# Kernel optimization log

Measured on AMD Instinct MI355X. Metric: run time of the kernel, lower is better.

Reference implementation:

```python
import jax, jax.numpy as jnp
import numpy as np

HIDDEN = 32


def setup_inputs() -> dict:
    key = jax.random.key(0)
    ks = jax.random.split(key, 8)
    B, T, I = 1024, 512, 64
    s_ih = 1.0 / np.sqrt(HIDDEN)
    return {
        "x": jax.random.normal(ks[0], (B, T, I), dtype=jnp.float32),
        "h0": jnp.zeros((1, B, HIDDEN), dtype=jnp.float32),
        "W_ih": jax.random.uniform(ks[1], (HIDDEN, I), jnp.float32, -s_ih, s_ih),
        "b_ih": jax.random.uniform(ks[2], (HIDDEN,), jnp.float32, -s_ih, s_ih),
        "W_hh": jax.random.uniform(ks[3], (HIDDEN, HIDDEN), jnp.float32, -s_ih, s_ih),
        "b_hh": jax.random.uniform(ks[4], (HIDDEN,), jnp.float32, -s_ih, s_ih),
        "W_out": jax.random.uniform(ks[5], (1, HIDDEN), jnp.float32, -s_ih, s_ih),
        "b_out": jax.random.uniform(ks[6], (1,), jnp.float32, -s_ih, s_ih),
    }


def reference(x, h0, W_ih, b_ih, W_hh, b_hh, W_out, b_out):
    # x: [B, T, I]; h0: [1, B, H] (num_layers=1)
    # Precompute input contribution for all timesteps in one GEMM: [B, T, H]
    x_proj = jnp.einsum("bti,hi->bth", x, W_ih) + b_ih

    def step(h, xt):  # h: [B, H], xt: [B, H]
        h_new = jnp.tanh(xt + h @ W_hh.T + b_hh)
        return h_new, h_new

    h_last, r_out_t = jax.lax.scan(step, h0[0], jnp.swapaxes(x_proj, 0, 1))
    r_out = jnp.swapaxes(r_out_t, 0, 1)  # [B, T, H]
    # Per-timestep Linear(32 -> 1), batched as one GEMM: [B, T, 1]
    outs = r_out @ W_out.T + b_out
    return outs, h_last[None]
```

## Files before the change

### kernel.cpp

```cpp
#include <hip/hip_runtime.h>

#define Bc 1024
#define Tc 512
#define Ic 64
#define Hc 32
#define XP 516

typedef __bf16 bf16x8 __attribute__((ext_vector_type(8)));
typedef __bf16 bf16x4 __attribute__((ext_vector_type(4)));
typedef float  f32x4  __attribute__((ext_vector_type(4)));

__device__ inline bf16x8 to_bf16x8(float4 u0, float4 u1) {
    bf16x8 t;
    t[0] = (__bf16)u0.x; t[1] = (__bf16)u0.y; t[2] = (__bf16)u0.z; t[3] = (__bf16)u0.w;
    t[4] = (__bf16)u1.x; t[5] = (__bf16)u1.y; t[6] = (__bf16)u1.z; t[7] = (__bf16)u1.w;
    return t;
}

#define RWC(hvv, wvv)                                                         \
    a0 = fmaf((hvv).x, (wvv).x, a0);                                          \
    a1 = fmaf((hvv).y, (wvv).y, a1);                                          \
    a2 = fmaf((hvv).z, (wvv).z, a2);                                          \
    a3 = fmaf((hvv).w, (wvv).w, a3);

#define STEP(xval, uu)                                                        \
    {                                                                         \
        hbuf[half][h] = hval;                                                 \
        __builtin_amdgcn_wave_barrier();                                      \
        const float4* hv = (const float4*)hbuf[half];                         \
        const float4 h0v = hv[0], h1v = hv[1], h2v = hv[2], h3v = hv[3],      \
                     h4v = hv[4], h5v = hv[5], h6v = hv[6], h7v = hv[7];      \
        float a0 = (xval) + bias, a1 = 0.f, a2 = 0.f, a3 = 0.f;               \
        RWC(h0v, w0) RWC(h1v, w1) RWC(h2v, w2) RWC(h3v, w3)                   \
        RWC(h4v, w4) RWC(h5v, w5) RWC(h6v, w6) RWC(h7v, w7)                   \
        const float a = (a0 + a1) + (a2 + a3);                                \
        const float p  = __builtin_amdgcn_exp2f(a * 2.8853900817779268f);     \
        const float rr = __builtin_amdgcn_rcpf(p + 1.0f);                     \
        hval = fmaf(-2.0f, rr, 1.0f);                                         \
        pbuf[half][uu][h] = wo * hval;                                        \
        __builtin_amdgcn_wave_barrier();                                      \
    }

#define CVT4(dst, src)                                                        \
    dst.x = (float)(src)[0]; dst.y = (float)(src)[1];                         \
    dst.z = (float)(src)[2]; dst.w = (float)(src)[3];

__global__ __launch_bounds__(64) void fused_rnn_kernel(
    const float* __restrict__ x, const float* __restrict__ Wih,
    const float* __restrict__ bih, const float* __restrict__ h0,
    const float* __restrict__ Whh, const float* __restrict__ bhh,
    const float* __restrict__ Wout, const float* __restrict__ bout,
    float* __restrict__ out)
{
    __shared__ __bf16 xq[2][Hc][XP];
    __shared__ float hbuf[2][32];
    __shared__ float pbuf[2][16][34];

    const int lane = threadIdx.x;
    const int half = lane >> 5;
    const int h    = lane & 31;
    const int m    = lane & 15;
    const int q    = lane >> 4;
    const int b0   = blockIdx.x * 2;

    bf16x8 Bf[2][2];
#pragma unroll
    for (int nh = 0; nh < 2; ++nh)
#pragma unroll
        for (int kh = 0; kh < 2; ++kh) {
            const float* wp = Wih + (m + 16 * nh) * Ic + q * 8 + kh * 32;
            Bf[nh][kh] = to_bf16x8(((const float4*)wp)[0], ((const float4*)wp)[1]);
        }
    const float bias0 = bih[m];
    const float bias1 = bih[m + 16];

#pragma unroll 4
    for (int tt = 0; tt < 64; ++tt) {
        const int bb = tt >> 5;
        const int lt = tt & 31;
        const float* xp0 =
            x + ((size_t)(b0 + bb) * Tc + lt * 16 + m) * Ic + q * 8;
        const bf16x8 A0 = to_bf16x8(((const float4*)xp0)[0],
                                    ((const float4*)xp0)[1]);
        const bf16x8 A1 = to_bf16x8(((const float4*)(xp0 + 32))[0],
                                    ((const float4*)(xp0 + 32))[1]);

        f32x4 acc0 = {0.f, 0.f, 0.f, 0.f};
        f32x4 acc1 = {0.f, 0.f, 0.f, 0.f};
        acc0 = __builtin_amdgcn_mfma_f32_16x16x32_bf16(A0, Bf[0][0], acc0, 0, 0, 0);
        acc0 = __builtin_amdgcn_mfma_f32_16x16x32_bf16(A1, Bf[0][1], acc0, 0, 0, 0);
        acc1 = __builtin_amdgcn_mfma_f32_16x16x32_bf16(A0, Bf[1][0], acc1, 0, 0, 0);
        acc1 = __builtin_amdgcn_mfma_f32_16x16x32_bf16(A1, Bf[1][1], acc1, 0, 0, 0);

        bf16x4 p0, p1;
        p0[0] = (__bf16)(acc0[0] + bias0); p0[1] = (__bf16)(acc0[1] + bias0);
        p0[2] = (__bf16)(acc0[2] + bias0); p0[3] = (__bf16)(acc0[3] + bias0);
        p1[0] = (__bf16)(acc1[0] + bias1); p1[1] = (__bf16)(acc1[1] + bias1);
        p1[2] = (__bf16)(acc1[2] + bias1); p1[3] = (__bf16)(acc1[3] + bias1);
        *(bf16x4*)&xq[bb][m][lt * 16 + q * 4]      = p0;
        *(bf16x4*)&xq[bb][m + 16][lt * 16 + q * 4] = p1;
    }

    __syncthreads();

    const float4* wrow = (const float4*)(Whh + h * Hc);
    const float4 w0 = wrow[0], w1 = wrow[1], w2 = wrow[2], w3 = wrow[3],
                 w4 = wrow[4], w5 = wrow[5], w6 = wrow[6], w7 = wrow[7];
    const float bias = bhh[h];
    const float wo   = Wout[h];
    const float bo   = bout[0];

    float hval = h0[(size_t)(b0 + half) * Hc + h];
    float* orow = out + (size_t)(b0 + half) * Tc;

    const __bf16* xrow = &xq[half][h][0];

    bf16x4 r0 = *(const bf16x4*)(xrow + 0), r1 = *(const bf16x4*)(xrow + 4),
           r2 = *(const bf16x4*)(xrow + 8), r3 = *(const bf16x4*)(xrow + 12);
    float4 q0, q1, q2, q3;
    CVT4(q0, r0) CVT4(q1, r1) CVT4(q2, r2) CVT4(q3, r3)

    for (int tb = 0; tb < Tc / 16; ++tb) {
        const int tbn = (tb + 1 < Tc / 16) ? tb + 1 : tb;
        const __bf16* nx = xrow + tbn * 16;
        const bf16x4 m0 = *(const bf16x4*)(nx + 0),
                     m1 = *(const bf16x4*)(nx + 4),
                     m2 = *(const bf16x4*)(nx + 8),
                     m3 = *(const bf16x4*)(nx + 12);

        STEP(q0.x, 0)  STEP(q0.y, 1)  STEP(q0.z, 2)  STEP(q0.w, 3)
        STEP(q1.x, 4)  STEP(q1.y, 5)  STEP(q1.z, 6)  STEP(q1.w, 7)
        STEP(q2.x, 8)  STEP(q2.y, 9)  STEP(q2.z, 10) STEP(q2.w, 11)
        STEP(q3.x, 12) STEP(q3.y, 13) STEP(q3.z, 14) STEP(q3.w, 15)

        __builtin_amdgcn_wave_barrier();

        if (h < 16) {
            const float2* pr = (const float2*)pbuf[half][h];
            float2 sa = pr[0], sb = pr[1];
#pragma unroll
            for (int mm = 2; mm < 16; mm += 2) {
                sa.x += pr[mm].x;     sa.y += pr[mm].y;
                sb.x += pr[mm + 1].x; sb.y += pr[mm + 1].y;
            }
            orow[tb * 16 + h] = ((sa.x + sb.x) + (sa.y + sb.y)) + bo;
        }
        __builtin_amdgcn_wave_barrier();

        CVT4(q0, m0) CVT4(q1, m1) CVT4(q2, m2) CVT4(q3, m3)
    }

    out[(size_t)Bc * Tc + (size_t)(b0 + half) * Hc + h] = hval;
}

extern "C" void kernel_launch(void* const* d_in, const int* in_sizes, int n_in,
                              void* d_out, int out_size, void* d_ws, size_t ws_size,
                              hipStream_t stream) {
    const float* x    = (const float*)d_in[0];
    const float* h0   = (const float*)d_in[1];
    const float* Wih  = (const float*)d_in[2];
    const float* bih  = (const float*)d_in[3];
    const float* Whh  = (const float*)d_in[4];
    const float* bhh  = (const float*)d_in[5];
    const float* Wout = (const float*)d_in[6];
    const float* bout = (const float*)d_in[7];
    float* out = (float*)d_out;

    fused_rnn_kernel<<<Bc / 2, 64, 0, stream>>>(x, Wih, bih, h0, Whh, bhh,
                                                Wout, bout, out);
}
```

Before: 275.5 us.

## Warp-specialize RNN: MFMA recurrence over 16 batches with producer wave for input projection

Replaces the scalar per-lane recurrence (two batches per block, FMA dot products through LDS) with a two-wave design. One wave runs the hidden-state recurrence for 16 batch rows as f16 MFMAs, using a sigmoid reformulation of tanh and permlane swaps to rebuild the B operand in registers. The other wave streams x, computes the input projection with bf16 MFMAs into a triple-buffered LDS ring and writes the reduced outputs. This targets the serial per-step latency and the low occupancy of the old layout, at the cost of f16 precision in the recurrence and one block-wide barrier per 8 timesteps.

```diff
diff --git a/kernel.cpp b/kernel.cpp
--- a/kernel.cpp
+++ b/kernel.cpp
@@ -4,11 +4,17 @@
 #define Tc 512
 #define Ic 64
 #define Hc 32
-#define XP 516
-
-typedef __bf16 bf16x8 __attribute__((ext_vector_type(8)));
-typedef __bf16 bf16x4 __attribute__((ext_vector_type(4)));
-typedef float  f32x4  __attribute__((ext_vector_type(4)));
+#define NB 16
+#define TT 8
+#define NT (Tc / TT)
+#define XP2 36
+#define L2E2 2.8853900817779268f
+
+typedef __bf16   bf16x8 __attribute__((ext_vector_type(8)));
+typedef _Float16 half8  __attribute__((ext_vector_type(8)));
+typedef float    f32x4  __attribute__((ext_vector_type(4)));
+typedef unsigned u32x4  __attribute__((ext_vector_type(4)));
+typedef unsigned uint2v __attribute__((ext_vector_type(2)));
 
 __device__ inline bf16x8 to_bf16x8(float4 u0, float4 u1) {
     bf16x8 t;
@@ -16,141 +22,279 @@
     t[4] = (__bf16)u1.x; t[5] = (__bf16)u1.y; t[6] = (__bf16)u1.z; t[7] = (__bf16)u1.w;
     return t;
 }
-
-#define RWC(hvv, wvv)                                                         \
-    a0 = fmaf((hvv).x, (wvv).x, a0);                                          \
-    a1 = fmaf((hvv).y, (wvv).y, a1);                                          \
-    a2 = fmaf((hvv).z, (wvv).z, a2);                                          \
-    a3 = fmaf((hvv).w, (wvv).w, a3);
-
-#define STEP(xval, uu)                                                        \
+__device__ inline bf16x8 to_bf16x8s(float4 u0, float4 u1, float s) {
+    bf16x8 t;
+    t[0] = (__bf16)(u0.x*s); t[1] = (__bf16)(u0.y*s); t[2] = (__bf16)(u0.z*s); t[3] = (__bf16)(u0.w*s);
+    t[4] = (__bf16)(u1.x*s); t[5] = (__bf16)(u1.y*s); t[6] = (__bf16)(u1.z*s); t[7] = (__bf16)(u1.w*s);
+    return t;
+}
+
+
+#if __has_builtin(__builtin_amdgcn_permlane16_swap)
+#define PLSWAP(A, B)                                                          \
+    { uint2v _t = __builtin_amdgcn_permlane16_swap((A), (B), false, false);   \
+      (A) = _t[0]; (B) = _t[1]; }
+#else
+#define PLSWAP(A, B)                                                          \
+    asm("s_nop 1\n\tv_permlane16_swap_b32 %0, %1" : "+v"(A), "+v"(B));
+#endif
+#if __has_builtin(__builtin_amdgcn_permlane32_swap)
+#define P32SWAP(A, B)                                                         \
+    { uint2v _t = __builtin_amdgcn_permlane32_swap((A), (B), false, false);   \
+      (A) = _t[0]; (B) = _t[1]; }
+#else
+#define P32SWAP(A, B)                                                         \
+    asm("s_nop 1\n\tv_permlane32_swap_b32 %0, %1" : "+v"(A), "+v"(B));
+#endif
+
+#define RSW16(X, OUT) { unsigned a__=(X), b__=(X); PLSWAP(a__,b__); OUT = ps16 ? a__ : b__; }
+#define RSW32(X, OUT) { unsigned a__=(X), b__=(X); P32SWAP(a__,b__); OUT = ps32 ? a__ : b__; }
+
+#define PK(a, b) __builtin_bit_cast(unsigned, __builtin_amdgcn_cvt_pkrtz((a), (b)))
+
+#define SSTEP(CC1, CC2, CN1, CN2, uu, tpf, upf)                               \
     {                                                                         \
-        hbuf[half][h] = hval;                                                 \
-        __builtin_amdgcn_wave_barrier();                                      \
-        const float4* hv = (const float4*)hbuf[half];                         \
-        const float4 h0v = hv[0], h1v = hv[1], h2v = hv[2], h3v = hv[3],      \
-                     h4v = hv[4], h5v = hv[5], h6v = hv[6], h7v = hv[7];      \
-        float a0 = (xval) + bias, a1 = 0.f, a2 = 0.f, a3 = 0.f;               \
-        RWC(h0v, w0) RWC(h1v, w1) RWC(h2v, w2) RWC(h3v, w3)                   \
-        RWC(h4v, w4) RWC(h5v, w5) RWC(h6v, w6) RWC(h7v, w7)                   \
-        const float a = (a0 + a1) + (a2 + a3);                                \
-        const float p  = __builtin_amdgcn_exp2f(a * 2.8853900817779268f);     \
-        const float rr = __builtin_amdgcn_rcpf(p + 1.0f);                     \
-        hval = fmaf(-2.0f, rr, 1.0f);                                         \
-        pbuf[half][uu][h] = wo * hval;                                        \
-        __builtin_amdgcn_wave_barrier();                                      \
-    }
-
-#define CVT4(dst, src)                                                        \
-    dst.x = (float)(src)[0]; dst.y = (float)(src)[1];                         \
-    dst.z = (float)(src)[2]; dst.w = (float)(src)[3];
-
-__global__ __launch_bounds__(64) void fused_rnn_kernel(
+        const float* pf_ = xqlds + (((tpf) % 3) * TT + (upf)) * (NB * XP2)    \
+                           + n * XP2 + 4 * q;                                 \
+        CN1 = *(const f32x4*)pf_;                                             \
+        CN2 = *(const f32x4*)(pf_ + 16);                                      \
+        const f32x4 D1_ = __builtin_amdgcn_mfma_f32_16x16x32_f16(A1f, Bst, CC1, 0, 0, 0); \
+        const f32x4 D2_ = __builtin_amdgcn_mfma_f32_16x16x32_f16(A2f, Bst, CC2, 0, 0, 0); \
+        r10 = __builtin_amdgcn_rcpf(__builtin_amdgcn_exp2f(D1_[0]) + 1.0f);   \
+        r11 = __builtin_amdgcn_rcpf(__builtin_amdgcn_exp2f(D1_[1]) + 1.0f);   \
+        r12 = __builtin_amdgcn_rcpf(__builtin_amdgcn_exp2f(D1_[2]) + 1.0f);   \
+        r13 = __builtin_amdgcn_rcpf(__builtin_amdgcn_exp2f(D1_[3]) + 1.0f);   \
+        r20 = __builtin_amdgcn_rcpf(__builtin_amdgcn_exp2f(D2_[0]) + 1.0f);   \
+        r21 = __builtin_amdgcn_rcpf(__builtin_amdgcn_exp2f(D2_[1]) + 1.0f);   \
+        r22 = __builtin_amdgcn_rcpf(__builtin_amdgcn_exp2f(D2_[2]) + 1.0f);   \
+        r23 = __builtin_amdgcn_rcpf(__builtin_amdgcn_exp2f(D2_[3]) + 1.0f);   \
+        const unsigned G0_ = PK(r10, r20), G1_ = PK(r11, r21);                \
+        const unsigned G2_ = PK(r12, r22), G3_ = PK(r13, r23);                \
+        unsigned B1_, B2_, B3_;                                               \
+        RSW16(G1_, B1_) RSW32(G2_, B2_) RSW16(G3_, B3_)                       \
+        u32x4 bu_; bu_[0] = G0_; bu_[1] = B1_; bu_[2] = B2_; bu_[3] = B3_;    \
+        Bst = __builtin_bit_cast(half8, bu_);                                 \
+        pbuf[(((tb & 1) * TT + (uu)) * NB + n) * 4 + q] =                     \
+            fmaf(r10, w2a0, fmaf(r11, w2a1, fmaf(r12, w2a2, fmaf(r13, w2a3,  \
+            fmaf(r20, w2b0, fmaf(r21, w2b1, fmaf(r22, w2b2, r23 * w2b3)))))));\
+    }
+
+#define XDECL(S) float4 X##S##0, X##S##1, X##S##2, X##S##3;
+
+#define HLOAD(S, wt)                                                          \
+    if ((wt) < Tc) {                                                          \
+        const float* xp_ = x + ((size_t)(b0 + n) * Tc + (wt)) * Ic + q * 8;   \
+        X##S##0 = ((const float4*)xp_)[0];                                    \
+        X##S##1 = ((const float4*)xp_)[1];                                    \
+        X##S##2 = ((const float4*)(xp_ + 32))[0];                             \
+        X##S##3 = ((const float4*)(xp_ + 32))[1];                             \
+    }
+
+#define HMFMA(S, wt)                                                          \
+    if ((wt) < Tc) {                                                          \
+        const bf16x8 A0_ = to_bf16x8(X##S##0, X##S##1);                       \
+        const bf16x8 A1_ = to_bf16x8(X##S##2, X##S##3);                       \
+        f32x4 d1_ = CbH1, d2_ = CbH2;                                         \
+        d1_ = __builtin_amdgcn_mfma_f32_16x16x32_bf16(A0_, Pw00, d1_, 0,0,0); \
+        d1_ = __builtin_amdgcn_mfma_f32_16x16x32_bf16(A1_, Pw01, d1_, 0,0,0); \
+        d2_ = __builtin_amdgcn_mfma_f32_16x16x32_bf16(A0_, Pw10, d2_, 0,0,0); \
+        d2_ = __builtin_amdgcn_mfma_f32_16x16x32_bf16(A1_, Pw11, d2_, 0,0,0); \
+        float* wb_ = xqlds + ((((wt) >> 3) % 3) * TT + ((wt) & 7)) * (NB * XP2); \
+        wb_[(4*q + 0) * XP2 + n]      = d1_[0];                               \
+        wb_[(4*q + 1) * XP2 + n]      = d1_[1];                               \
+        wb_[(4*q + 2) * XP2 + n]      = d1_[2];                               \
+        wb_[(4*q + 3) * XP2 + n]      = d1_[3];                               \
+        wb_[(4*q + 0) * XP2 + n + 16] = d2_[0];                               \
+        wb_[(4*q + 1) * XP2 + n + 16] = d2_[1];                               \
+        wb_[(4*q + 2) * XP2 + n + 16] = d2_[2];                               \
+        wb_[(4*q + 3) * XP2 + n + 16] = d2_[3];                               \
+    }
+
+#define HSTEP(S, wt, wtn) HMFMA(S, wt) HLOAD(S, wtn)
+
+#define HRED(tbr)                                                             \
+    {                                                                         \
+        const int n2_ = lane >> 2, ug_ = (lane & 3) * 2;                      \
+        const float* pr_ = pbuf + ((((tbr) & 1) * TT + ug_) * NB + n2_) * 4;  \
+        const f32x4 pa_ = *(const f32x4*)pr_;                                 \
+        const f32x4 pb_ = *(const f32x4*)(pr_ + NB * 4);                      \
+        float2 sv_;                                                           \
+        sv_.x = ((pa_[0] + pa_[1]) + (pa_[2] + pa_[3])) + cst;                \
+        sv_.y = ((pb_[0] + pb_[1]) + (pb_[2] + pb_[3])) + cst;                \
+        *(float2*)(out + (size_t)(b0 + n2_) * Tc + (tbr) * TT + ug_) = sv_;   \
+    }
+
+__global__ __launch_bounds__(128, 1) void fused_rnn_kernel(
     const float* __restrict__ x, const float* __restrict__ Wih,
     const float* __restrict__ bih, const float* __restrict__ h0,
     const float* __restrict__ Whh, const float* __restrict__ bhh,
     const float* __restrict__ Wout, const float* __restrict__ bout,
     float* __restrict__ out)
 {
-    __shared__ __bf16 xq[2][Hc][XP];
-    __shared__ float hbuf[2][32];
-    __shared__ float pbuf[2][16][34];
-
-    const int lane = threadIdx.x;
-    const int half = lane >> 5;
-    const int h    = lane & 31;
-    const int m    = lane & 15;
+    __shared__ float xqlds[3 * TT * NB * XP2];
+    __shared__ float pbuf[2 * TT * NB * 4];
+
+    const int tid  = threadIdx.x;
+    const int wid  = tid >> 6;
+    const int lane = tid & 63;
+    const int n    = lane & 15;
     const int q    = lane >> 4;
-    const int b0   = blockIdx.x * 2;
-
-    bf16x8 Bf[2][2];
-#pragma unroll
-    for (int nh = 0; nh < 2; ++nh)
-#pragma unroll
-        for (int kh = 0; kh < 2; ++kh) {
-            const float* wp = Wih + (m + 16 * nh) * Ic + q * 8 + kh * 32;
-            Bf[nh][kh] = to_bf16x8(((const float4*)wp)[0], ((const float4*)wp)[1]);
-        }
-    const float bias0 = bih[m];
-    const float bias1 = bih[m + 16];
-
-#pragma unroll 4
-    for (int tt = 0; tt < 64; ++tt) {
-        const int bb = tt >> 5;
-        const int lt = tt & 31;
-        const float* xp0 =
-            x + ((size_t)(b0 + bb) * Tc + lt * 16 + m) * Ic + q * 8;
-        const bf16x8 A0 = to_bf16x8(((const float4*)xp0)[0],
-                                    ((const float4*)xp0)[1]);
-        const bf16x8 A1 = to_bf16x8(((const float4*)(xp0 + 32))[0],
-                                    ((const float4*)(xp0 + 32))[1]);
-
-        f32x4 acc0 = {0.f, 0.f, 0.f, 0.f};
-        f32x4 acc1 = {0.f, 0.f, 0.f, 0.f};
-        acc0 = __builtin_amdgcn_mfma_f32_16x16x32_bf16(A0, Bf[0][0], acc0, 0, 0, 0);
-        acc0 = __builtin_amdgcn_mfma_f32_16x16x32_bf16(A1, Bf[0][1], acc0, 0, 0, 0);
-        acc1 = __builtin_amdgcn_mfma_f32_16x16x32_bf16(A0, Bf[1][0], acc1, 0, 0, 0);
-        acc1 = __builtin_amdgcn_mfma_f32_16x16x32_bf16(A1, Bf[1][1], acc1, 0, 0, 0);
-
-        bf16x4 p0, p1;
-        p0[0] = (__bf16)(acc0[0] + bias0); p0[1] = (__bf16)(acc0[1] + bias0);
-        p0[2] = (__bf16)(acc0[2] + bias0); p0[3] = (__bf16)(acc0[3] + bias0);
-        p1[0] = (__bf16)(acc1[0] + bias1); p1[1] = (__bf16)(acc1[1] + bias1);
-        p1[2] = (__bf16)(acc1[2] + bias1); p1[3] = (__bf16)(acc1[3] + bias1);
-        *(bf16x4*)&xq[bb][m][lt * 16 + q * 4]      = p0;
-        *(bf16x4*)&xq[bb][m + 16][lt * 16 + q * 4] = p1;
-    }
-
+    const int b0   = blockIdx.x * NB;
+
+    bool ps16 = false, ps32 = false;
+    half8 A1f = {}, A2f = {}, Bst = {};
+    f32x4 Ca1 = {}, Ca2 = {}, Cb1 = {}, Cb2 = {};
+    float w2a0=0,w2a1=0,w2a2=0,w2a3=0,w2b0=0,w2b1=0,w2b2=0,w2b3=0;
+    float r10=0,r11=0,r12=0,r13=0,r20=0,r21=0,r22=0,r23=0;
+    bf16x8 Pw00, Pw01, Pw10, Pw11;
+    f32x4 CbH1 = {}, CbH2 = {};
+    float cst = 0.f;
+    XDECL(0) XDECL(1) XDECL(2) XDECL(3) XDECL(4) XDECL(5) XDECL(6) XDECL(7)
+
+    if (wid == 1) {
+#pragma unroll
+        for (int hh = 0; hh < 2; ++hh)
+#pragma unroll
+            for (int kh = 0; kh < 2; ++kh) {
+                const float* wp = Wih + (n + 16 * hh) * Ic + q * 8 + kh * 32;
+                const bf16x8 f = to_bf16x8s(((const float4*)wp)[0],
+                                            ((const float4*)wp)[1], L2E2);
+                if (hh == 0 && kh == 0) Pw00 = f;
+                else if (hh == 0)       Pw01 = f;
+                else if (kh == 0)       Pw10 = f;
+                else                    Pw11 = f;
+            }
+        float rs1 = 0.f, rs2 = 0.f;
+        {
+            const float4* wr1 = (const float4*)(Whh + n * Hc);
+            const float4* wr2 = (const float4*)(Whh + (n + 16) * Hc);
+#pragma unroll
+            for (int j = 0; j < 8; ++j) {
+                const float4 a = wr1[j], b = wr2[j];
+                rs1 += (a.x + a.y) + (a.z + a.w);
+                rs2 += (b.x + b.y) + (b.z + b.w);
+            }
+        }
+        const float cb1 = (bih[n] + bhh[n] + rs1) * L2E2;
+        const float cb2 = (bih[n + 16] + bhh[n + 16] + rs2) * L2E2;
+        CbH1[0] = cb1; CbH1[1] = cb1; CbH1[2] = cb1; CbH1[3] = cb1;
+        CbH2[0] = cb2; CbH2[1] = cb2; CbH2[2] = cb2; CbH2[3] = cb2;
+        {
+            const float4* wo4 = (const float4*)Wout;
+            float s = 0.f;
+#pragma unroll
+            for (int j = 0; j < 8; ++j) {
+                const float4 a = wo4[j];
+                s += (a.x + a.y) + (a.z + a.w);
+            }
+            cst = s + bout[0];
+        }
+        HLOAD(0, 0) HLOAD(1, 1) HLOAD(2, 2) HLOAD(3, 3)
+        HLOAD(4, 4) HLOAD(5, 5) HLOAD(6, 6) HLOAD(7, 7)
+        HSTEP(0, 0, 8)  HSTEP(1, 1, 9)  HSTEP(2, 2, 10) HSTEP(3, 3, 11)
+        HSTEP(4, 4, 12) HSTEP(5, 5, 13) HSTEP(6, 6, 14) HSTEP(7, 7, 15)
+        HSTEP(0, 8, 16)  HSTEP(1, 9, 17)  HSTEP(2, 10, 18) HSTEP(3, 11, 19)
+        HSTEP(4, 12, 20) HSTEP(5, 13, 21) HSTEP(6, 14, 22) HSTEP(7, 15, 23)
+    } else {
+        {
+            unsigned d0 = (unsigned)lane, d1 = (unsigned)lane;
+            PLSWAP(d0, d1)
+            ps16 = (d0 == (unsigned)(lane ^ 16));
+            unsigned e0 = (unsigned)lane, e1 = (unsigned)lane;
+            P32SWAP(e0, e1)
+            ps32 = (e0 == (unsigned)(lane ^ 32));
+        }
+        u32x4 Bsv;
+        {
+            const unsigned g0 = (unsigned)(4*q + 0) | ((unsigned)(16 + 4*q + 0) << 16);
+            const unsigned g1 = (unsigned)(4*q + 1) | ((unsigned)(16 + 4*q + 1) << 16);
+            const unsigned g2 = (unsigned)(4*q + 2) | ((unsigned)(16 + 4*q + 2) << 16);
+            const unsigned g3 = (unsigned)(4*q + 3) | ((unsigned)(16 + 4*q + 3) << 16);
+            unsigned s1, s2, s3;
+            RSW16(g1, s1) RSW32(g2, s2) RSW16(g3, s3)
+            Bsv[0] = g0; Bsv[1] = s1; Bsv[2] = s2; Bsv[3] = s3;
+        }
+        {
+            const float cw = -2.0f * L2E2;
+            const float* w0r = Whh + n * Hc;
+            const float* w1r = Whh + (n + 16) * Hc;
+            u32x4 aw1, aw2;
+#pragma unroll
+            for (int jp = 0; jp < 4; ++jp) {
+                const unsigned lo = Bsv[jp] & 0xFFFFu, hi = Bsv[jp] >> 16;
+                aw1[jp] = PK(w0r[lo] * cw, w0r[hi] * cw);
+                aw2[jp] = PK(w1r[lo] * cw, w1r[hi] * cw);
+            }
+            A1f = __builtin_bit_cast(half8, aw1);
+            A2f = __builtin_bit_cast(half8, aw2);
+        }
+        w2a0 = -2.0f * Wout[4*q + 0]; w2a1 = -2.0f * Wout[4*q + 1];
+        w2a2 = -2.0f * Wout[4*q + 2]; w2a3 = -2.0f * Wout[4*q + 3];
+        w2b0 = -2.0f * Wout[16 + 4*q + 0]; w2b1 = -2.0f * Wout[16 + 4*q + 1];
+        w2b2 = -2.0f * Wout[16 + 4*q + 2]; w2b3 = -2.0f * Wout[16 + 4*q + 3];
+        {
+            const float* h0p = h0 + (size_t)(b0 + n) * Hc;
+            u32x4 bi;
+#pragma unroll
+            for (int jp = 0; jp < 4; ++jp) {
+                const unsigned lo = Bsv[jp] & 0xFFFFu, hi = Bsv[jp] >> 16;
+                bi[jp] = PK(fmaf(-0.5f, h0p[lo], 0.5f),
+                            fmaf(-0.5f, h0p[hi], 0.5f));
+            }
+            Bst = __builtin_bit_cast(half8, bi);
+            r10 = fmaf(-0.5f, h0p[4*q + 0], 0.5f);
+            r11 = fmaf(-0.5f, h0p[4*q + 1], 0.5f);
+            r12 = fmaf(-0.5f, h0p[4*q + 2], 0.5f);
+            r13 = fmaf(-0.5f, h0p[4*q + 3], 0.5f);
+            r20 = fmaf(-0.5f, h0p[16 + 4*q + 0], 0.5f);
+            r21 = fmaf(-0.5f, h0p[16 + 4*q + 1], 0.5f);
+            r22 = fmaf(-0.5f, h0p[16 + 4*q + 2], 0.5f);
+            r23 = fmaf(-0.5f, h0p[16 + 4*q + 3], 0.5f);
+        }
+    }
     __syncthreads();
 
-    const float4* wrow = (const float4*)(Whh + h * Hc);
-    const float4 w0 = wrow[0], w1 = wrow[1], w2 = wrow[2], w3 = wrow[3],
-                 w4 = wrow[4], w5 = wrow[5], w6 = wrow[6], w7 = wrow[7];
-    const float bias = bhh[h];
-    const float wo   = Wout[h];
-    const float bo   = bout[0];
-
-    float hval = h0[(size_t)(b0 + half) * Hc + h];
-    float* orow = out + (size_t)(b0 + half) * Tc;
-
-    const __bf16* xrow = &xq[half][h][0];
-
-    bf16x4 r0 = *(const bf16x4*)(xrow + 0), r1 = *(const bf16x4*)(xrow + 4),
-           r2 = *(const bf16x4*)(xrow + 8), r3 = *(const bf16x4*)(xrow + 12);
-    float4 q0, q1, q2, q3;
-    CVT4(q0, r0) CVT4(q1, r1) CVT4(q2, r2) CVT4(q3, r3)
-
-    for (int tb = 0; tb < Tc / 16; ++tb) {
-        const int tbn = (tb + 1 < Tc / 16) ? tb + 1 : tb;
-        const __bf16* nx = xrow + tbn * 16;
-        const bf16x4 m0 = *(const bf16x4*)(nx + 0),
-                     m1 = *(const bf16x4*)(nx + 4),
-                     m2 = *(const bf16x4*)(nx + 8),
-                     m3 = *(const bf16x4*)(nx + 12);
-
-        STEP(q0.x, 0)  STEP(q0.y, 1)  STEP(q0.z, 2)  STEP(q0.w, 3)
-        STEP(q1.x, 4)  STEP(q1.y, 5)  STEP(q1.z, 6)  STEP(q1.w, 7)
-        STEP(q2.x, 8)  STEP(q2.y, 9)  STEP(q2.z, 10) STEP(q2.w, 11)
-        STEP(q3.x, 12) STEP(q3.y, 13) STEP(q3.z, 14) STEP(q3.w, 15)
-
-        __builtin_amdgcn_wave_barrier();
-
-        if (h < 16) {
-            const float2* pr = (const float2*)pbuf[half][h];
-            float2 sa = pr[0], sb = pr[1];
-#pragma unroll
-            for (int mm = 2; mm < 16; mm += 2) {
-                sa.x += pr[mm].x;     sa.y += pr[mm].y;
-                sb.x += pr[mm + 1].x; sb.y += pr[mm + 1].y;
-            }
-            orow[tb * 16 + h] = ((sa.x + sb.x) + (sa.y + sb.y)) + bo;
-        }
-        __builtin_amdgcn_wave_barrier();
-
-        CVT4(q0, m0) CVT4(q1, m1) CVT4(q2, m2) CVT4(q3, m3)
-    }
-
-    out[(size_t)Bc * Tc + (size_t)(b0 + half) * Hc + h] = hval;
+    if (wid == 0) {
+        const float* pf = xqlds + n * XP2 + 4 * q;
+        Ca1 = *(const f32x4*)pf;
+        Ca2 = *(const f32x4*)(pf + 16);
+    }
+
+#pragma unroll 1
+    for (int tb = 0; tb < NT; ++tb) {
+        if (wid == 0) {
+            const int tn = (tb + 1 < NT) ? tb + 1 : tb;
+            SSTEP(Ca1, Ca2, Cb1, Cb2, 0, tb, 1)
+            SSTEP(Cb1, Cb2, Ca1, Ca2, 1, tb, 2)
+            SSTEP(Ca1, Ca2, Cb1, Cb2, 2, tb, 3)
+            SSTEP(Cb1, Cb2, Ca1, Ca2, 3, tb, 4)
+            SSTEP(Ca1, Ca2, Cb1, Cb2, 4, tb, 5)
+            SSTEP(Cb1, Cb2, Ca1, Ca2, 5, tb, 6)
+            SSTEP(Ca1, Ca2, Cb1, Cb2, 6, tb, 7)
+            SSTEP(Cb1, Cb2, Ca1, Ca2, 7, tn, 0)
+        } else {
+            const int wb = (tb + 2) * TT, wl = (tb + 3) * TT;
+            HSTEP(0, wb + 0, wl + 0) HSTEP(1, wb + 1, wl + 1)
+            HSTEP(2, wb + 2, wl + 2) HSTEP(3, wb + 3, wl + 3)
+            HSTEP(4, wb + 4, wl + 4) HSTEP(5, wb + 5, wl + 5)
+            HSTEP(6, wb + 6, wl + 6) HSTEP(7, wb + 7, wl + 7)
+            if (tb >= 1) HRED(tb - 1)
+        }
+        __syncthreads();
+    }
+
+    if (wid == 1) {
+        HRED(NT - 1)
+    } else {
+        float* hl = out + (size_t)Bc * Tc + (size_t)(b0 + n) * Hc;
+        float4 v1, v2;
+        v1.x = fmaf(-2.0f, r10, 1.0f); v1.y = fmaf(-2.0f, r11, 1.0f);
+        v1.z = fmaf(-2.0f, r12, 1.0f); v1.w = fmaf(-2.0f, r13, 1.0f);
+        v2.x = fmaf(-2.0f, r20, 1.0f); v2.y = fmaf(-2.0f, r21, 1.0f);
+        v2.z = fmaf(-2.0f, r22, 1.0f); v2.w = fmaf(-2.0f, r23, 1.0f);
+        *(float4*)(hl + 4 * q)      = v1;
+        *(float4*)(hl + 16 + 4 * q) = v2;
+    }
 }
 
 extern "C" void kernel_launch(void* const* d_in, const int* in_sizes, int n_in,
@@ -166,6 +310,6 @@
     const float* bout = (const float*)d_in[7];
     float* out = (float*)d_out;
 
-    fused_rnn_kernel<<<Bc / 2, 64, 0, stream>>>(x, Wih, bih, h0, Whh, bhh,
-                                                Wout, bout, out);
+    fused_rnn_kernel<<<Bc / NB, 128, 0, stream>>>(x, Wih, bih, h0, Whh, bhh,
+                                                  Wout, bout, out);
 }
```

New measurement: 509.0 us. 84.8% more time.
